# Kernel tuning notes

Measured on AMD Instinct MI355X. Metric: run time of the kernel, lower is better.

## Reference

```python
import jax, jax.numpy as jnp
import numpy as np

WS = 8            # window_size
SHIFT = WS // 2   # cyclic shift
NHEADS = 6
EPS = 1e-5


def _rel_pos_index(ws):
    coords = np.stack(np.meshgrid(np.arange(ws), np.arange(ws), indexing='ij'))  # [2,ws,ws]
    flat = coords.reshape(2, -1)                       # [2,N]
    rel = flat[:, :, None] - flat[:, None, :]          # [2,N,N]
    rel = rel.transpose(1, 2, 0).copy()
    rel[:, :, 0] += ws - 1
    rel[:, :, 1] += ws - 1
    rel[:, :, 0] *= 2 * ws - 1
    return rel.sum(-1)                                 # [N,N] indices into bias table


def _attn_mask(H, W, ws, shift):
    # standard Swin boundary mask for the shifted configuration
    img = np.zeros((H, W))
    cnt = 0
    for hs in (slice(0, -ws), slice(-ws, -shift), slice(-shift, None)):
        for wsl in (slice(0, -ws), slice(-ws, -shift), slice(-shift, None)):
            img[hs, wsl] = cnt
            cnt += 1
    mw = img.reshape(H // ws, ws, W // ws, ws).transpose(0, 2, 1, 3).reshape(-1, ws * ws)
    m = mw[:, None, :] - mw[:, :, None]
    return np.where(m != 0, -100.0, 0.0).astype(np.float32)  # [nW, N, N]


def instance_norm(x):
    # InstanceNorm over spatial dims, no affine (torch default)
    m = x.mean(axis=(2, 3), keepdims=True)
    v = x.var(axis=(2, 3), keepdims=True)
    return (x - m) * jax.lax.rsqrt(v + EPS)


def setup_inputs() -> dict:
    key = jax.random.key(0)
    ks = jax.random.split(key, 8)
    B, C, H, W, E = 4, 192, 256, 256, 128
    s = 0.02
    return {
        'x': jax.random.normal(ks[0], (B, C, H, W), jnp.float32),
        'cond': jax.random.normal(ks[1], (B, E), jnp.float32),
        'qkv_w': jax.random.normal(ks[2], (3 * C, C), jnp.float32) * s,
        'qkv_b': jnp.zeros((3 * C,), jnp.float32),
        'proj_w': jax.random.normal(ks[3], (C, C), jnp.float32) * s,
        'proj_b': jnp.zeros((C,), jnp.float32),
        'rel_bias': jax.random.normal(ks[4], ((2 * WS - 1) ** 2, NHEADS), jnp.float32) * s,
        'film_w': jax.random.normal(ks[5], (2 * C, E), jnp.float32) * s,
        'film_b': jnp.zeros((2 * C,), jnp.float32),
    }


def shifted_window_attention(xn, qkv_w, qkv_b, proj_w, proj_b, rel_bias):
    B, C, H, W = xn.shape
    h, ws, shift = NHEADS, WS, SHIFT
    d = C // h
    N = ws * ws
    nW = (H // ws) * (W // ws)
    scale = d ** -0.5

    xs = jnp.transpose(xn, (0, 2, 3, 1))                         # BHWC
    xs = jnp.roll(xs, (-shift, -shift), axis=(1, 2))             # cyclic shift
    win = xs.reshape(B, H // ws, ws, W // ws, ws, C)
    win = win.transpose(0, 1, 3, 2, 4, 5).reshape(B * nW, N, C)  # window partition

    qkv = win @ qkv_w.T + qkv_b                                  # [Bn, N, 3C]
    q, k, v = [t.reshape(B * nW, N, h, d).transpose(0, 2, 1, 3)
               for t in jnp.split(qkv, 3, axis=-1)]              # [Bn, h, N, d]

    attn = jnp.einsum('bhnd,bhmd->bhnm', q, k) * scale           # [Bn, h, N, N]
    bias = rel_bias[_rel_pos_index(ws)].transpose(2, 0, 1)       # [h, N, N]
    attn = attn + bias[None]
    mask = jnp.asarray(_attn_mask(H, W, ws, shift))              # [nW, N, N]
    attn = attn.reshape(B, nW, h, N, N) + mask[None, :, None]
    attn = jax.nn.softmax(attn, axis=-1).reshape(B * nW, h, N, N)

    out = jnp.einsum('bhnm,bhmd->bhnd', attn, v)                 # [Bn, h, N, d]
    out = out.transpose(0, 2, 1, 3).reshape(B * nW, N, C)
    out = out @ proj_w.T + proj_b

    out = out.reshape(B, H // ws, W // ws, ws, ws, C)
    out = out.transpose(0, 1, 3, 2, 4, 5).reshape(B, H, W, C)    # window merge
    out = jnp.roll(out, (shift, shift), axis=(1, 2))             # reverse shift
    return jnp.transpose(out, (0, 3, 1, 2))                      # BCHW


def reference(x, cond, qkv_w, qkv_b, proj_w, proj_b, rel_bias, film_w, film_b):
    # branch 1: x + attn(norm1(x))
    xn = instance_norm(x)
    x = x + shifted_window_attention(xn, qkv_w, qkv_b, proj_w, proj_b, rel_bias)
    # branch 2: x + FiLM(norm2(x), cond)
    x2 = instance_norm(x)
    gb = cond @ film_w.T + film_b                                # [B, 2C]
    gamma, beta = jnp.split(gb, 2, axis=-1)
    x2 = x2 * gamma[:, :, None, None] + beta[:, :, None, None]
    return x + x2
```

## Files before the change

### kernel.cpp

```cpp
#include <hip/hip_runtime.h>

#define BATCH 4
#define CH    192
#define PLANE 65536

typedef unsigned short u16;
typedef unsigned char  u8;
typedef __bf16 bf16x8_t __attribute__((ext_vector_type(8)));
typedef unsigned short u16x8 __attribute__((ext_vector_type(8)));
typedef unsigned short u16x4 __attribute__((ext_vector_type(4)));
typedef float f32x4 __attribute__((ext_vector_type(4)));

__device__ __forceinline__ u16 f2bf(float f) {
  __bf16 h = (__bf16)f;
  return __builtin_bit_cast(u16, h);
}
__device__ __forceinline__ float bf2f(u16 h) {
  unsigned u = ((unsigned)h) << 16;
  return __builtin_bit_cast(float, u);
}
__device__ __forceinline__ f32x4 mfma16(u16x8 a, u16x8 b, f32x4 c) {
  return __builtin_amdgcn_mfma_f32_16x16x32_bf16(
      __builtin_bit_cast(bf16x8_t, a), __builtin_bit_cast(bf16x8_t, b), c, 0, 0, 0);
}

__global__ void stats_kernel(const float* __restrict__ in, float* __restrict__ st) {
  const int plane = blockIdx.x;
  const float4* p = (const float4*)(in + (long)plane * PLANE);
  float s = 0.f, ss = 0.f;
  for (int i = threadIdx.x; i < PLANE/4; i += 256) {
    float4 v = p[i];
    s  += v.x + v.y + v.z + v.w;
    ss += v.x*v.x + v.y*v.y + v.z*v.z + v.w*v.w;
  }
  for (int off = 1; off < 64; off <<= 1) {
    s  += __shfl_xor(s,  off, 64);
    ss += __shfl_xor(ss, off, 64);
  }
  __shared__ float aux[4][2];
  const int w = threadIdx.x >> 6;
  if ((threadIdx.x & 63) == 0) { aux[w][0] = s; aux[w][1] = ss; }
  __syncthreads();
  if (threadIdx.x == 0) {
    float S  = aux[0][0]+aux[1][0]+aux[2][0]+aux[3][0];
    float SS = aux[0][1]+aux[1][1]+aux[2][1]+aux[3][1];
    float mean = S * (1.f/PLANE);
    float var  = SS * (1.f/PLANE) - mean*mean;
    st[plane*2]   = mean;
    st[plane*2+1] = rsqrtf(var + 1e-5f);
  }
}

__global__ void cvt_kernel(const float* __restrict__ a, const float* __restrict__ b,
                           const float* __restrict__ rb,
                           u16* __restrict__ wa, u16* __restrict__ wb, u8* __restrict__ bq) {
  const int i = blockIdx.x*256 + threadIdx.x;
  if (i < 576*192) wa[i] = f2bf(a[i]);
  if (i < 192*192) wb[i] = f2bf(b[i]);
  if (i < 1350) {
    float v = fminf(fmaxf(rintf(rb[i]*128.f) + 128.f, 0.f), 255.f);
    bq[i] = (u8)v;
  }
}

__global__ void film_prep(const float* __restrict__ cond, const float* __restrict__ fw,
                          const float* __restrict__ fb, float* __restrict__ gb) {
  const int i = blockIdx.x*256 + threadIdx.x;
  if (i >= BATCH*384) return;
  const int bb = i / 384, oc = i - bb*384;
  const float* cw = fw + oc*128;
  const float* cv = cond + bb*128;
  float s = fb[oc];
  for (int k = 0; k < 128; ++k) s += cv[k]*cw[k];
  gb[i] = s;
}

__global__ __launch_bounds__(256) void prep_kernel(
    const float* __restrict__ x, const float* __restrict__ st, u16* __restrict__ xn)
{
  __shared__ u16 tile[32*264];
  const int t = threadIdx.x;
  const int bid = blockIdx.x;
  const int cc = bid % 6;
  const int wh = (bid/6) % 32;
  const int b  = bid / 192;
  const int c0 = cc*32;
  const int ww = t >> 3, ax = t & 7;
  const int gx = (ww*8 + ax + 4) & 255;
  const int gxb = gx & ~3, gxr = gx & 3;
  const long wid = b*1024 + wh*32 + ww;

  for (int ay = 0; ay < 8; ++ay) {
    const int gy = (wh*8 + ay + 4) & 255;
    for (int it = 0; it < 8; ++it) {
      const int id = it*256 + t;
      const int cl = id >> 6;
      const int px = (id & 63) << 2;
      const int c  = c0 + cl;
      const float m = st[(b*192+c)*2], r = st[(b*192+c)*2+1];
      float4 v = *(const float4*)(x + (((long)(b*192+c)) << 16) + gy*256 + px);
      u16x4 pk;
      pk[0] = f2bf((v.x-m)*r); pk[1] = f2bf((v.y-m)*r);
      pk[2] = f2bf((v.z-m)*r); pk[3] = f2bf((v.w-m)*r);
      *(u16x4*)&tile[cl*264 + (px ^ ((cl&7)<<2))] = pk;
    }
    __syncthreads();
    u16* dst = xn + wid*12288 + (ay*8+ax)*192 + c0;
    #pragma unroll
    for (int k = 0; k < 4; ++k) {
      u16x8 pk;
      #pragma unroll
      for (int e = 0; e < 8; ++e) {
        const int c = k*8 + e;
        pk[e] = tile[c*264 + (gxb ^ ((c&7)<<2)) + gxr];
      }
      *(u16x8*)(dst + k*8) = pk;
    }
    __syncthreads();
  }
}

__global__ __launch_bounds__(512, 4) void attn_kernel(
    const u16* __restrict__ xn, const u16* __restrict__ wq, const u16* __restrict__ wp,
    const float* __restrict__ qkvb, const float* __restrict__ projb,
    const u8* __restrict__ bq, u16* __restrict__ pw)
{
  __shared__ __attribute__((aligned(16))) unsigned char smem[70016];
  u16* Xs    = (u16*)smem;
  u16* G     = (u16*)(smem + 25600);
  u16* Vt    = (u16*)(smem + 43008);
  u16* Pout  = (u16*)(smem + 25600);
  u8*  biasQ = (u8*)(smem + 52224);
  u16* Ps    = (u16*)(smem + 53632);

  const int t    = threadIdx.x;
  const int lane = t & 63;
  const int wave = t >> 6;
  const int arow = lane & 15;
  const int kgrp = lane >> 4;

  const int bid = blockIdx.x;
  const int wid = (bid & 7) * 512 + (bid >> 3);
  const int b   = wid >> 10;
  const int wh  = (wid >> 5) & 31;
  const int ww  = wid & 31;

  const u16* src = xn + (long)wid*12288;
  #pragma unroll
  for (int it = 0; it < 3; ++it) {
    const int id = it*512 + t;
    const int row = id/24, c8 = (id%24)*8;
    *(u16x8*)&Xs[row*200 + c8] = *(const u16x8*)(src + id*8);
  }
  for (int i = t; i < 1350; i += 512) biasQ[i] = bq[i];
  __syncthreads();

  const int hh = wave >> 2;
  const int mt = wave & 3;
  u16x4 og[3][2];

  #pragma unroll
  for (int g = 0; g < 3; ++g) {
    for (int nt0 = wave; nt0 < 12; nt0 += 8) {
      f32x4 acc[4] = {{0,0,0,0},{0,0,0,0},{0,0,0,0},{0,0,0,0}};
      const int col = nt0*16 + arow;
      const int mat = col >> 6;
      const int ch  = mat*192 + g*64 + (col & 63);
      const u16* wrow = wq + ch*192 + kgrp*8;
      #pragma unroll
      for (int ks = 0; ks < 6; ++ks) {
        u16x8 bfr = *(const u16x8*)(wrow + ks*32);
        #pragma unroll
        for (int m = 0; m < 4; ++m) {
          u16x8 af = *(const u16x8*)&Xs[(m*16+arow)*200 + ks*32 + kgrp*8];
          acc[m] = mfma16(af, bfr, acc[m]);
        }
      }
      const float addb = qkvb[ch];
      if (mat == 2) {
        const int vc = col & 63;
        #pragma unroll
        for (int m = 0; m < 4; ++m) {
          u16x4 pk;
          #pragma unroll
          for (int r = 0; r < 4; ++r) pk[r] = f2bf(acc[m][r] + addb);
          *(u16x4*)&Vt[vc*72 + m*16 + kgrp*4] = pk;
        }
      } else {
        const float mult = (mat == 0) ? 0.17677669529663687f : 1.0f;
        const int gc = mat*64 + (col & 63);
        #pragma unroll
        for (int m = 0; m < 4; ++m)
          #pragma unroll
          for (int r = 0; r < 4; ++r)
            G[(m*16 + kgrp*4 + r)*136 + gc] = f2bf((acc[m][r] + addb)*mult);
      }
    }
    __syncthreads();

    const int hd = g*2 + hh;
    u16x8 qf = *(const u16x8*)&G[(mt*16+arow)*136 + hh*32 + kgrp*8];
    f32x4 sv[4];
    #pragma unroll
    for (int nt = 0; nt < 4; ++nt) {
      u16x8 kf = *(const u16x8*)&G[(nt*16+arow)*136 + 64 + hh*32 + kgrp*8];
      f32x4 z = {0,0,0,0};
      sv[nt] = mfma16(qf, kf, z);
    }

    float p[4][4];
    #pragma unroll
    for (int r = 0; r < 4; ++r) {
      const int i  = mt*16 + kgrp*4 + r;
      const int iy = i >> 3, ix = i & 7;
      const int ri = ((wh==31) ? (iy<4?1:2) : 0)*3 + ((ww==31) ? (ix<4?1:2) : 0);
      #pragma unroll
      for (int nt = 0; nt < 4; ++nt) {
        const int j  = nt*16 + arow;
        const int jy = j >> 3, jx = j & 7;
        const int rj = ((wh==31) ? (jy<4?1:2) : 0)*3 + ((ww==31) ? (jx<4?1:2) : 0);
        const int bidx = ((iy-jy+7)*15 + (ix-jx+7))*6 + hd;
        float s = sv[nt][r] + (float)((int)biasQ[bidx] - 128) * 0.0078125f;
        if (ri != rj) s -= 100.0f;
        p[nt][r] = s;
      }
    }
    #pragma unroll
    for (int r = 0; r < 4; ++r) {
      float mx = fmaxf(fmaxf(p[0][r], p[1][r]), fmaxf(p[2][r], p[3][r]));
      for (int off = 1; off < 16; off <<= 1) mx = fmaxf(mx, __shfl_xor(mx, off, 64));
      float sum = 0.f;
      #pragma unroll
      for (int nt = 0; nt < 4; ++nt) { p[nt][r] = __expf(p[nt][r] - mx); sum += p[nt][r]; }
      for (int off = 1; off < 16; off <<= 1) sum += __shfl_xor(sum, off, 64);
      const float inv = 1.0f / sum;
      #pragma unroll
      for (int nt = 0; nt < 4; ++nt) p[nt][r] *= inv;
    }
    u16* myP = Ps + wave*1024;
    #pragma unroll
    for (int r = 0; r < 4; ++r) {
      const int i = kgrp*4 + r;
      #pragma unroll
      for (int nt = 0; nt < 4; ++nt) {
        const int j = nt*16 + arow;
        myP[i*64 + ((j + 8*i) & 63)] = f2bf(p[nt][r]);
      }
    }
    f32x4 oacc[2] = {{0,0,0,0},{0,0,0,0}};
    #pragma unroll
    for (int ks = 0; ks < 2; ++ks) {
      u16x8 pf = *(const u16x8*)&myP[arow*64 + ((ks*32 + kgrp*8 + 8*arow) & 63)];
      #pragma unroll
      for (int nt = 0; nt < 2; ++nt) {
        u16x8 vf = *(const u16x8*)&Vt[(hh*32 + nt*16 + arow)*72 + ks*32 + kgrp*8];
        oacc[nt] = mfma16(pf, vf, oacc[nt]);
      }
    }
    #pragma unroll
    for (int nt = 0; nt < 2; ++nt)
      #pragma unroll
      for (int r = 0; r < 4; ++r)
        og[g][nt][r] = f2bf(oacc[nt][r]);
    __syncthreads();
  }

  #pragma unroll
  for (int g = 0; g < 3; ++g)
    #pragma unroll
    for (int nt = 0; nt < 2; ++nt) {
      const int colb = g*64 + hh*32 + nt*16 + arow;
      #pragma unroll
      for (int r = 0; r < 4; ++r)
        Xs[(mt*16 + kgrp*4 + r)*200 + colb] = og[g][nt][r];
    }
  __syncthreads();

  for (int nt0 = wave; nt0 < 12; nt0 += 8) {
    const int ch = nt0*16 + arow;
    const float pb = projb[ch];
    f32x4 acc[4];
    #pragma unroll
    for (int m = 0; m < 4; ++m) { f32x4 v = {pb,pb,pb,pb}; acc[m] = v; }
    const u16* wrow = wp + ch*192 + kgrp*8;
    #pragma unroll
    for (int ks = 0; ks < 6; ++ks) {
      u16x8 bfr = *(const u16x8*)(wrow + ks*32);
      #pragma unroll
      for (int m = 0; m < 4; ++m) {
        u16x8 af = *(const u16x8*)&Xs[(m*16+arow)*200 + ks*32 + kgrp*8];
        acc[m] = mfma16(af, bfr, acc[m]);
      }
    }
    #pragma unroll
    for (int m = 0; m < 4; ++m) {
      u16x4 pk;
      #pragma unroll
      for (int r = 0; r < 4; ++r) pk[r] = f2bf(acc[m][r]);
      *(u16x4*)&Pout[ch*72 + m*16 + kgrp*4] = pk;
    }
  }
  __syncthreads();

  u16* dstw = pw + (long)wid*12288;
  #pragma unroll
  for (int it = 0; it < 3; ++it) {
    const int id = it*512 + t;
    const int c = id >> 3, tk8 = (id & 7)*8;
    *(u16x8*)(dstw + c*64 + tk8) = *(const u16x8*)&Pout[c*72 + tk8];
  }
}

__global__ __launch_bounds__(256) void merge_kernel(
    const float* __restrict__ x, u16* __restrict__ pw, float2* __restrict__ part2)
{
  __shared__ float2 pc[4][32];
  const int t = threadIdx.x;
  const int bid = blockIdx.x;
  const int cc = bid % 6;
  const int wh = (bid/6) % 32;
  const int b  = bid / 192;
  const int c0 = cc*32;
  const int ww = t >> 3, sub = t & 7;
  const int wave = t >> 6;
  const long wid = b*1024 + wh*32 + ww;
  u16* pwin = pw + wid*12288;
  const int gy  = (wh*8 + sub + 4) & 255;
  const int gx0 = (ww*8 + 4) & 255;
  const int gxB = (ww*8 + 8) & 255;

  for (int c = 0; c < 32; ++c) {
    const float* xr = x + (((long)(b*192 + c0 + c)) << 16) + gy*256;
    float4 xa = *(const float4*)(xr + gx0);
    float4 xb = *(const float4*)(xr + gxB);
    u16* pv = pwin + (c0 + c)*64 + sub*8;
    u16x8 pr = *(const u16x8*)pv;
    float v0 = xa.x + bf2f(pr[0]);
    float v1 = xa.y + bf2f(pr[1]);
    float v2 = xa.z + bf2f(pr[2]);
    float v3 = xa.w + bf2f(pr[3]);
    float v4 = xb.x + bf2f(pr[4]);
    float v5 = xb.y + bf2f(pr[5]);
    float v6 = xb.z + bf2f(pr[6]);
    float v7 = xb.w + bf2f(pr[7]);
    u16x8 vb;
    vb[0]=f2bf(v0); vb[1]=f2bf(v1); vb[2]=f2bf(v2); vb[3]=f2bf(v3);
    vb[4]=f2bf(v4); vb[5]=f2bf(v5); vb[6]=f2bf(v6); vb[7]=f2bf(v7);
    *(u16x8*)pv = vb;
    float s = v0+v1+v2+v3+v4+v5+v6+v7;
    float q = v0*v0+v1*v1+v2*v2+v3*v3+v4*v4+v5*v5+v6*v6+v7*v7;
    for (int off = 1; off < 64; off <<= 1) {
      s += __shfl_xor(s, off, 64);
      q += __shfl_xor(q, off, 64);
    }
    if ((t & 63) == 0) { float2 v = {s, q}; pc[wave][c] = v; }
  }
  __syncthreads();
  if (t < 32) {
    float2 a0 = pc[0][t], a1 = pc[1][t], a2 = pc[2][t], a3 = pc[3][t];
    float2 o = {a0.x+a1.x+a2.x+a3.x, a0.y+a1.y+a2.y+a3.y};
    part2[wh*768 + b*192 + c0 + t] = o;
  }
}

__global__ __launch_bounds__(256) void stats2R_kernel(
    const float2* __restrict__ part2, float2* __restrict__ st2f) {
  const int i = blockIdx.x*256 + threadIdx.x;
  if (i >= 768) return;
  float s = 0.f, q = 0.f;
  for (int wh = 0; wh < 32; ++wh) {
    float2 v = part2[wh*768 + i];
    s += v.x; q += v.y;
  }
  const float mean = s * (1.f/PLANE);
  const float var  = q * (1.f/PLANE) - mean*mean;
  float2 o = {mean, rsqrtf(var + 1e-5f)};
  st2f[i] = o;
}

__global__ __launch_bounds__(256) void final_kernel(
    const u16* __restrict__ pw, const float2* __restrict__ st2f,
    const float* __restrict__ gb, float* __restrict__ out)
{
  __shared__ u16 tile[32*264];
  const int t = threadIdx.x;
  const int bid = blockIdx.x;
  const int lin = (bid & 7)*768 + (bid >> 3);
  const int cc = lin % 6;
  const int rowid = lin / 6;
  const int gy = rowid & 255;
  const int b  = rowid >> 8;
  const int c0 = cc*32;
  const int gys = (gy + 252) & 255;
  const int wh = gys >> 3, ay = gys & 7;

  {
    const int ww = t >> 3, cq = t & 7;
    const long wid = b*1024 + wh*32 + ww;
    const u16* srcw = pw + wid*12288;
    const int g1 = ww*8 + 4, g2 = (ww*8 + 8) & 255;
    #pragma unroll
    for (int j = 0; j < 4; ++j) {
      const int c = cq*4 + j;
      u16x8 v = *(const u16x8*)(srcw + (c0+c)*64 + ay*8);
      const int sw = (c & 7) << 2;
      u16x4 lo = {v[0],v[1],v[2],v[3]}, hi = {v[4],v[5],v[6],v[7]};
      *(u16x4*)&tile[c*264 + (g1 ^ sw)] = lo;
      *(u16x4*)&tile[c*264 + (g2 ^ sw)] = hi;
    }
  }
  __syncthreads();

  const int cl = t >> 3, seg = t & 7;
  const int c = c0 + cl;
  const float2 mr = st2f[b*192 + c];
  const float mean = mr.x, rstd = mr.y;
  const float gmm  = gb[b*384 + c];
  const float be   = gb[b*384 + 192 + c];
  const long base = (((long)(b*192 + c)) << 16) + gy*256 + seg*32;
  float* orow = out + base;
  const int sw = (cl & 7) << 2;
  #pragma unroll
  for (int q4 = 0; q4 < 32; q4 += 4) {
    const int px = seg*32 + q4;
    u16x4 pv = *(const u16x4*)&tile[cl*264 + (px ^ sw)];
    float4 o;
    float v0 = bf2f(pv[0]), v1 = bf2f(pv[1]), v2 = bf2f(pv[2]), v3 = bf2f(pv[3]);
    o.x = v0 + (v0 - mean)*rstd*gmm + be;
    o.y = v1 + (v1 - mean)*rstd*gmm + be;
    o.z = v2 + (v2 - mean)*rstd*gmm + be;
    o.w = v3 + (v3 - mean)*rstd*gmm + be;
    *(float4*)(orow + q4) = o;
  }
}

extern "C" void kernel_launch(void* const* d_in, const int* in_sizes, int n_in,
                              void* d_out, int out_size, void* d_ws, size_t ws_size,
                              hipStream_t stream) {
  const float* x      = (const float*)d_in[0];
  const float* cond   = (const float*)d_in[1];
  const float* qkv_w  = (const float*)d_in[2];
  const float* qkv_b  = (const float*)d_in[3];
  const float* proj_w = (const float*)d_in[4];
  const float* proj_b = (const float*)d_in[5];
  const float* relb   = (const float*)d_in[6];
  const float* film_w = (const float*)d_in[7];
  const float* film_b = (const float*)d_in[8];
  float* out = (float*)d_out;

  char* ws = (char*)d_ws;
  float*  stats1 = (float*)ws;
  float2* st2f   = (float2*)(ws + 6144);
  float*  gb     = (float*)(ws + 12288);
  u16*    wq     = (u16*)(ws + 18432);
  u16*    wp     = (u16*)(ws + 239616);
  u8*     bqq    = (u8*)(ws + 313344);
  u16*    xbuf   = (u16*)(ws + 362496);
  float2* part2  = (float2*)(ws + 362496 + 100663296);

  stats_kernel<<<768, 256, 0, stream>>>(x, stats1);
  cvt_kernel<<<432, 256, 0, stream>>>(qkv_w, proj_w, relb, wq, wp, bqq);
  film_prep<<<6, 256, 0, stream>>>(cond, film_w, film_b, gb);
  prep_kernel<<<768, 256, 0, stream>>>(x, stats1, xbuf);
  attn_kernel<<<4096, 512, 0, stream>>>(xbuf, wq, wp, qkv_b, proj_b, bqq, xbuf);
  merge_kernel<<<768, 256, 0, stream>>>(x, xbuf, part2);
  stats2R_kernel<<<3, 256, 0, stream>>>(part2, st2f);
  final_kernel<<<6144, 256, 0, stream>>>(xbuf, st2f, gb, out);
}
```

Baseline: 538.2 us.

## Fuse residual merge and norm2 partial stats into attention kernel

The attention kernel now rebuilds the raw input from its normalized bf16 window using the stage-1 mean and std, adds the projection output, writes the residual, and emits per-window sum and sum-of-squares. This removes the separate merge kernel, which re-read x in fp32 and re-read and rewrote the window buffer. A new stats2 kernel reduces the per-window partials. The bias/mask path also gains a fast branch for non-boundary windows. The cost is that the residual uses a de-normalized bf16 input rather than the original fp32 x, which adds precision error.

Result: faster. 505.7 us (-6.0%).

```diff
diff --git a/kernel.cpp b/kernel.cpp
--- a/kernel.cpp
+++ b/kernel.cpp
@@ -123,15 +123,17 @@
 __global__ __launch_bounds__(512, 4) void attn_kernel(
     const u16* __restrict__ xn, const u16* __restrict__ wq, const u16* __restrict__ wp,
     const float* __restrict__ qkvb, const float* __restrict__ projb,
-    const u8* __restrict__ bq, u16* __restrict__ pw)
+    const u8* __restrict__ bq, const float* __restrict__ st,
+    u16* __restrict__ pw, float2* __restrict__ part)
 {
-  __shared__ __attribute__((aligned(16))) unsigned char smem[70016];
-  u16* Xs    = (u16*)smem;
-  u16* G     = (u16*)(smem + 25600);
-  u16* Vt    = (u16*)(smem + 43008);
-  u16* Pout  = (u16*)(smem + 25600);
-  u8*  biasQ = (u8*)(smem + 52224);
-  u16* Ps    = (u16*)(smem + 53632);
+  __shared__ __attribute__((aligned(16))) unsigned char smem[71504];
+  u16*    Xs    = (u16*)smem;
+  u16*    G     = (u16*)(smem + 25600);
+  u16*    Vt    = (u16*)(smem + 43008);
+  u16*    Pout  = (u16*)(smem + 25600);
+  u8*     biasQ = (u8*)(smem + 52224);
+  float2* stp   = (float2*)(smem + 53576);
+  u16*    Ps    = (u16*)(smem + 55120);
 
   const int t    = threadIdx.x;
   const int lane = t & 63;
@@ -153,10 +155,17 @@
     *(u16x8*)&Xs[row*200 + c8] = *(const u16x8*)(src + id*8);
   }
   for (int i = t; i < 1350; i += 512) biasQ[i] = bq[i];
+  for (int i = t; i < 192; i += 512) {
+    const float mean = st[(b*192+i)*2];
+    const float rstd = st[(b*192+i)*2 + 1];
+    float2 o = {mean, 1.0f / rstd};
+    stp[i] = o;
+  }
   __syncthreads();
 
   const int hh = wave >> 2;
   const int mt = wave & 3;
+  const bool boundary = (wh == 31) || (ww == 31);
   u16x4 og[3][2];
 
   #pragma unroll
@@ -208,21 +217,38 @@
       sv[nt] = mfma16(qf, kf, z);
     }
 
+    int qj6[4];
+    #pragma unroll
+    for (int nt = 0; nt < 4; ++nt) {
+      const int j = nt*16 + arow;
+      qj6[nt] = ((j>>3)*15 + (j&7))*6;
+    }
     float p[4][4];
-    #pragma unroll
-    for (int r = 0; r < 4; ++r) {
-      const int i  = mt*16 + kgrp*4 + r;
-      const int iy = i >> 3, ix = i & 7;
-      const int ri = ((wh==31) ? (iy<4?1:2) : 0)*3 + ((ww==31) ? (ix<4?1:2) : 0);
-      #pragma unroll
-      for (int nt = 0; nt < 4; ++nt) {
-        const int j  = nt*16 + arow;
-        const int jy = j >> 3, jx = j & 7;
-        const int rj = ((wh==31) ? (jy<4?1:2) : 0)*3 + ((ww==31) ? (jx<4?1:2) : 0);
-        const int bidx = ((iy-jy+7)*15 + (ix-jx+7))*6 + hd;
-        float s = sv[nt][r] + (float)((int)biasQ[bidx] - 128) * 0.0078125f;
-        if (ri != rj) s -= 100.0f;
-        p[nt][r] = s;
+    if (!boundary) {
+      #pragma unroll
+      for (int r = 0; r < 4; ++r) {
+        const int i = mt*16 + kgrp*4 + r;
+        const int qib = ((i>>3)*15 + (i&7) + 112)*6 + hd;
+        #pragma unroll
+        for (int nt = 0; nt < 4; ++nt)
+          p[nt][r] = sv[nt][r] + (float)((int)biasQ[qib - qj6[nt]] - 128) * 0.0078125f;
+      }
+    } else {
+      #pragma unroll
+      for (int r = 0; r < 4; ++r) {
+        const int i  = mt*16 + kgrp*4 + r;
+        const int iy = i >> 3, ix = i & 7;
+        const int qib = (iy*15 + ix + 112)*6 + hd;
+        const int ri = ((wh==31) ? (iy<4?1:2) : 0)*3 + ((ww==31) ? (ix<4?1:2) : 0);
+        #pragma unroll
+        for (int nt = 0; nt < 4; ++nt) {
+          const int j  = nt*16 + arow;
+          const int jy = j >> 3, jx = j & 7;
+          const int rj = ((wh==31) ? (jy<4?1:2) : 0)*3 + ((ww==31) ? (jx<4?1:2) : 0);
+          float sc = sv[nt][r] + (float)((int)biasQ[qib - qj6[nt]] - 128) * 0.0078125f;
+          if (ri != rj) sc -= 100.0f;
+          p[nt][r] = sc;
+        }
       }
     }
     #pragma unroll
@@ -265,6 +291,22 @@
     __syncthreads();
   }
 
+  u16x8 rawreg[3];
+  #pragma unroll
+  for (int it = 0; it < 3; ++it) {
+    const int id = it*512 + t;
+    const int c = id >> 3, tk8 = (id & 7)*8;
+    const float2 mi = stp[c];
+    u16x8 rr;
+    #pragma unroll
+    for (int e = 0; e < 8; ++e) {
+      float nv = bf2f(Xs[(tk8 + e)*200 + c]);
+      rr[e] = f2bf(nv*mi.y + mi.x);
+    }
+    rawreg[it] = rr;
+  }
+  __syncthreads();
+
   #pragma unroll
   for (int g = 0; g < 3; ++g)
     #pragma unroll
@@ -307,75 +349,52 @@
   for (int it = 0; it < 3; ++it) {
     const int id = it*512 + t;
     const int c = id >> 3, tk8 = (id & 7)*8;
-    *(u16x8*)(dstw + c*64 + tk8) = *(const u16x8*)&Pout[c*72 + tk8];
-  }
-}
-
-__global__ __launch_bounds__(256) void merge_kernel(
-    const float* __restrict__ x, u16* __restrict__ pw, float2* __restrict__ part2)
-{
-  __shared__ float2 pc[4][32];
-  const int t = threadIdx.x;
-  const int bid = blockIdx.x;
-  const int cc = bid % 6;
-  const int wh = (bid/6) % 32;
-  const int b  = bid / 192;
-  const int c0 = cc*32;
-  const int ww = t >> 3, sub = t & 7;
-  const int wave = t >> 6;
-  const long wid = b*1024 + wh*32 + ww;
-  u16* pwin = pw + wid*12288;
-  const int gy  = (wh*8 + sub + 4) & 255;
-  const int gx0 = (ww*8 + 4) & 255;
-  const int gxB = (ww*8 + 8) & 255;
-
-  for (int c = 0; c < 32; ++c) {
-    const float* xr = x + (((long)(b*192 + c0 + c)) << 16) + gy*256;
-    float4 xa = *(const float4*)(xr + gx0);
-    float4 xb = *(const float4*)(xr + gxB);
-    u16* pv = pwin + (c0 + c)*64 + sub*8;
-    u16x8 pr = *(const u16x8*)pv;
-    float v0 = xa.x + bf2f(pr[0]);
-    float v1 = xa.y + bf2f(pr[1]);
-    float v2 = xa.z + bf2f(pr[2]);
-    float v3 = xa.w + bf2f(pr[3]);
-    float v4 = xb.x + bf2f(pr[4]);
-    float v5 = xb.y + bf2f(pr[5]);
-    float v6 = xb.z + bf2f(pr[6]);
-    float v7 = xb.w + bf2f(pr[7]);
+    u16x8 pv = *(const u16x8*)&Pout[c*72 + tk8];
+    u16x8 rr = rawreg[it];
     u16x8 vb;
-    vb[0]=f2bf(v0); vb[1]=f2bf(v1); vb[2]=f2bf(v2); vb[3]=f2bf(v3);
-    vb[4]=f2bf(v4); vb[5]=f2bf(v5); vb[6]=f2bf(v6); vb[7]=f2bf(v7);
-    *(u16x8*)pv = vb;
-    float s = v0+v1+v2+v3+v4+v5+v6+v7;
-    float q = v0*v0+v1*v1+v2*v2+v3*v3+v4*v4+v5*v5+v6*v6+v7*v7;
-    for (int off = 1; off < 64; off <<= 1) {
-      s += __shfl_xor(s, off, 64);
-      q += __shfl_xor(q, off, 64);
-    }
-    if ((t & 63) == 0) { float2 v = {s, q}; pc[wave][c] = v; }
-  }
-  __syncthreads();
-  if (t < 32) {
-    float2 a0 = pc[0][t], a1 = pc[1][t], a2 = pc[2][t], a3 = pc[3][t];
-    float2 o = {a0.x+a1.x+a2.x+a3.x, a0.y+a1.y+a2.y+a3.y};
-    part2[wh*768 + b*192 + c0 + t] = o;
-  }
-}
-
-__global__ __launch_bounds__(256) void stats2R_kernel(
-    const float2* __restrict__ part2, float2* __restrict__ st2f) {
-  const int i = blockIdx.x*256 + threadIdx.x;
-  if (i >= 768) return;
+    float s = 0.f, q = 0.f;
+    #pragma unroll
+    for (int e = 0; e < 8; ++e) {
+      float v = bf2f(rr[e]) + bf2f(pv[e]);
+      vb[e] = f2bf(v);
+      s += v; q += v*v;
+    }
+    *(u16x8*)(dstw + c*64 + tk8) = vb;
+    s += __shfl_xor(s, 1, 64); q += __shfl_xor(q, 1, 64);
+    s += __shfl_xor(s, 2, 64); q += __shfl_xor(q, 2, 64);
+    s += __shfl_xor(s, 4, 64); q += __shfl_xor(q, 4, 64);
+    if ((lane & 7) == 0) {
+      float2 pr = {s, q};
+      part[(long)wid*192 + c] = pr;
+    }
+  }
+}
+
+__global__ __launch_bounds__(256) void stats2_kernel(
+    const float2* __restrict__ part, float2* __restrict__ st2f) {
+  const int b = blockIdx.x / 12, cg = blockIdx.x % 12;
+  const int cl = threadIdx.x & 15;
+  const int w0 = threadIdx.x >> 4;
+  const int c = cg*16 + cl;
   float s = 0.f, q = 0.f;
-  for (int wh = 0; wh < 32; ++wh) {
-    float2 v = part2[wh*768 + i];
+  for (int w = w0; w < 1024; w += 16) {
+    float2 v = part[((long)(b*1024 + w))*192 + c];
     s += v.x; q += v.y;
   }
-  const float mean = s * (1.f/PLANE);
-  const float var  = q * (1.f/PLANE) - mean*mean;
-  float2 o = {mean, rsqrtf(var + 1e-5f)};
-  st2f[i] = o;
+  s += __shfl_xor(s, 16, 64); q += __shfl_xor(q, 16, 64);
+  s += __shfl_xor(s, 32, 64); q += __shfl_xor(q, 32, 64);
+  __shared__ float2 aux[4][16];
+  if ((threadIdx.x & 63) < 16) { float2 v = {s, q}; aux[threadIdx.x >> 6][cl] = v; }
+  __syncthreads();
+  if (threadIdx.x < 16) {
+    float2 a0 = aux[0][cl], a1 = aux[1][cl], a2 = aux[2][cl], a3 = aux[3][cl];
+    float S = a0.x + a1.x + a2.x + a3.x;
+    float Q = a0.y + a1.y + a2.y + a3.y;
+    float mean = S * (1.f/PLANE);
+    float var  = Q * (1.f/PLANE) - mean*mean;
+    float2 o = {mean, rsqrtf(var + 1e-5f)};
+    st2f[b*192 + c] = o;
+  }
 }
 
 __global__ __launch_bounds__(256) void final_kernel(
@@ -456,14 +475,13 @@
   u16*    wp     = (u16*)(ws + 239616);
   u8*     bqq    = (u8*)(ws + 313344);
   u16*    xbuf   = (u16*)(ws + 362496);
-  float2* part2  = (float2*)(ws + 362496 + 100663296);
+  float2* part   = (float2*)(ws + 362496 + 100663296);
 
   stats_kernel<<<768, 256, 0, stream>>>(x, stats1);
   cvt_kernel<<<432, 256, 0, stream>>>(qkv_w, proj_w, relb, wq, wp, bqq);
   film_prep<<<6, 256, 0, stream>>>(cond, film_w, film_b, gb);
   prep_kernel<<<768, 256, 0, stream>>>(x, stats1, xbuf);
-  attn_kernel<<<4096, 512, 0, stream>>>(xbuf, wq, wp, qkv_b, proj_b, bqq, xbuf);
-  merge_kernel<<<768, 256, 0, stream>>>(x, xbuf, part2);
-  stats2R_kernel<<<3, 256, 0, stream>>>(part2, st2f);
+  attn_kernel<<<4096, 512, 0, stream>>>(xbuf, wq, wp, qkv_b, proj_b, bqq, stats1, xbuf, part);
+  stats2_kernel<<<48, 256, 0, stream>>>(part, st2f);
   final_kernel<<<6144, 256, 0, stream>>>(xbuf, st2f, gb, out);
 }
```
